# Performance work log

Hardware: AMD Instinct MI355X
Metric: run time of the kernel (lower is better)

Reference implementation:

```python
import jax, jax.numpy as jnp
import numpy as np

V, E, H = 50257, 512, 1024  # vocab, embed_dim, hidden_dim
B, S = 64, 2048             # batch, src_len


def setup_inputs() -> dict:
    key = jax.random.key(0)
    ks = jax.random.split(key, 16)
    sc = 0.02
    emb = jax.random.normal(ks[0], (V, E), jnp.float32) * sc
    emb = emb.at[0].set(0.0)  # padding_idx=0
    return {
        "x": jax.random.randint(ks[1], (B, 1), 0, V),
        "hidden": jax.random.normal(ks[2], (1, B, H), jnp.float32),
        "cell": jax.random.normal(ks[3], (1, B, H), jnp.float32),
        "encoder_outputs": jax.random.normal(ks[4], (B, S, H), jnp.float32),
        "emb": emb,
        "Wa_w": jax.random.normal(ks[5], (H, H), jnp.float32) * sc,
        "Wa_b": jnp.zeros((H,), jnp.float32),
        "Ua_w": jax.random.normal(ks[6], (H, H), jnp.float32) * sc,
        "Ua_b": jnp.zeros((H,), jnp.float32),
        "va_w": jax.random.normal(ks[7], (1, H), jnp.float32) * sc,
        "va_b": jnp.zeros((1,), jnp.float32),
        "Wih": jax.random.normal(ks[8], (4 * H, E + H), jnp.float32) * sc,
        "Whh": jax.random.normal(ks[9], (4 * H, H), jnp.float32) * sc,
        "bih": jnp.zeros((4 * H,), jnp.float32),
        "bhh": jnp.zeros((4 * H,), jnp.float32),
        "fc_w": jax.random.normal(ks[10], (V, H), jnp.float32) * sc,
        "fc_b": jnp.zeros((V,), jnp.float32),
    }


def reference(x, hidden, cell, encoder_outputs, emb, Wa_w, Wa_b, Ua_w, Ua_b,
              va_w, va_b, Wih, Whh, bih, bhh, fc_w, fc_b):
    # Embedding lookup: [B,1] -> [B,E]
    embedded = emb[x[:, 0]]
    # Bahdanau additive attention
    s_t = hidden[-1]                                          # [B,H]
    proj_s = jnp.einsum('bh,oh->bo', s_t, Wa_w) + Wa_b        # [B,H]
    proj_e = jnp.einsum('bsh,oh->bso', encoder_outputs, Ua_w) + Ua_b  # [B,S,H]
    e = jnp.tanh(proj_s[:, None, :] + proj_e)                 # [B,S,H]
    scores = jnp.einsum('bsh,h->bs', e, va_w[0]) + va_b[0]    # [B,S]
    attn = jax.nn.softmax(scores, axis=1)                     # [B,S]
    context = jnp.einsum('bs,bsh->bh', attn, encoder_outputs)  # [B,H]
    # Single-step LSTM (torch gate order: i, f, g, o)
    lstm_in = jnp.concatenate([embedded, context], axis=1)    # [B,E+H]
    gates = lstm_in @ Wih.T + bih + s_t @ Whh.T + bhh         # [B,4H]
    i, f, g, o = jnp.split(gates, 4, axis=1)
    i, f, o = jax.nn.sigmoid(i), jax.nn.sigmoid(f), jax.nn.sigmoid(o)
    g = jnp.tanh(g)
    c_new = f * cell[-1] + i * g
    h_new = o * jnp.tanh(c_new)
    predictions = (h_new @ fc_w.T + fc_b)[:, None, :]          # [B,1,V]
    return predictions, h_new[None], c_new[None]
```

## Files before the change

### kernel.cpp

```cpp
#include <hip/hip_runtime.h>
#include <hip/hip_bf16.h>

#define V_ 50257
#define H_ 1024
#define S_ 2048

typedef float f32x4 __attribute__((ext_vector_type(4)));
typedef short s16x8 __attribute__((ext_vector_type(8)));

__device__ __forceinline__ unsigned short f2bf(float f){
  unsigned u = __builtin_bit_cast(unsigned, f);
  return (unsigned short)((u + 0x7FFFu + ((u >> 16) & 1u)) >> 16);
}
__device__ __forceinline__ unsigned cvt2(float a, float b){
  return (unsigned)f2bf(a) | ((unsigned)f2bf(b) << 16);
}
__device__ __forceinline__ float bf2f(unsigned short h){
  return __builtin_bit_cast(float, (unsigned)h << 16);
}
__device__ __forceinline__ float fast_tanh(float x){
  return 1.0f - 2.0f/(__expf(2.0f*x)+1.0f);
}
__device__ __forceinline__ float fast_sig(float x){
  return 1.0f/(1.0f+__expf(-x));
}
__device__ __forceinline__ void gld_lds16(const void* g, void* l){
  __builtin_amdgcn_global_load_lds((const __attribute__((address_space(1))) void*)g,
                                   (__attribute__((address_space(3))) void*)l, 16, 0, 0);
}

#define BAR() do { __builtin_amdgcn_sched_barrier(0); __builtin_amdgcn_s_barrier(); __builtin_amdgcn_sched_barrier(0); } while(0)
#define VMW8() asm volatile("s_waitcnt vmcnt(8)" ::: "memory")
#define VMW0() asm volatile("s_waitcnt vmcnt(0)" ::: "memory")

__global__ __launch_bounds__(256) void k_cvt_bf16(const float* __restrict__ src,
                                                  unsigned short* __restrict__ dst, int n){
  int i = (blockIdx.x*256 + threadIdx.x)*4;
  if (i < n){
    float4 f = *(const float4*)(src + i);
    uint2 u;
    u.x = cvt2(f.x, f.y);
    u.y = cvt2(f.z, f.w);
    *(uint2*)(dst + i) = u;
  }
}

__global__ __launch_bounds__(256) void k_cvt_enc(const float* __restrict__ src,
                                                 unsigned short* __restrict__ dst){
  const size_t stride = (size_t)gridDim.x * 256;
  const float4* s4 = (const float4*)src;
  uint2* d2 = (uint2*)dst;
  for (size_t i = (size_t)blockIdx.x*256 + threadIdx.x; i < 33554432u; i += stride){
    float4 f = s4[i];
    uint2 u;
    u.x = cvt2(f.x, f.y);
    u.y = cvt2(f.z, f.w);
    d2[i] = u;
  }
}

__global__ __launch_bounds__(512,1) void k_proje256(
    const unsigned short* __restrict__ A,
    const unsigned short* __restrict__ Bw,
    const float* __restrict__ ps,
    const float* __restrict__ Ua_b,
    const float* __restrict__ va,
    float* __restrict__ part)
{
  extern __shared__ unsigned short smem[];
  const int t = threadIdx.x;
  const int lane = t & 63, wid = t >> 6;
  const int lr = lane & 15, lk = lane >> 4;
  const int wr = wid >> 2, wc = wid & 3;

  int bid = blockIdx.x;
  int L = (bid & 7) * 256 + (bid >> 3);
  const int wgm = L >> 2, wgn = L & 3;
  const int m0 = wgm * 256, n0 = wgn * 256;

  const int srow = lane >> 3;
  const int schunk = (lane & 7) ^ srow;

  f32x4 acc[8][4] = {};
  s16x8 af[4], bfr[4];

  auto STAGE = [&](int slot, int kt){
    #pragma unroll
    for (int h = 0; h < 4; ++h){
      const unsigned short* gsrc = (h < 2) ? A : Bw;
      const size_t g0 = (h < 2) ? (size_t)m0 : (size_t)n0;
      unsigned short* ldst = smem + ((h < 2) ? 0 : 32768) + slot*16384;
      #pragma unroll
      for (int j = 0; j < 2; ++j){
        int rb = (h & 1)*128 + j*64 + wid*8;
        gld_lds16(gsrc + (g0 + rb + srow)*1024 + kt*64 + schunk*8,
                  ldst + rb*64);
      }
    }
  };

#define SUBPH(As_, Bs_, msel, ks, LOADB) do { \
    if (LOADB){ \
      _Pragma("unroll") \
      for (int ni = 0; ni < 4; ++ni){ \
        int rl = wc*64 + ni*16 + lr; \
        bfr[ni] = *(const s16x8*)((Bs_) + rl*64 + ((((ks)*4+lk) ^ (lr&7))*8)); \
      } \
    } \
    _Pragma("unroll") \
    for (int mi = 0; mi < 4; ++mi){ \
      int rl = wr*128 + ((msel)*4+mi)*16 + lr; \
      af[mi] = *(const s16x8*)((As_) + rl*64 + ((((ks)*4+lk) ^ (lr&7))*8)); \
    } \
    __builtin_amdgcn_s_setprio(1); \
    _Pragma("unroll") \
    for (int mi = 0; mi < 4; ++mi) \
      _Pragma("unroll") \
      for (int ni = 0; ni < 4; ++ni) \
        acc[(msel)*4+mi][ni] = __builtin_amdgcn_mfma_f32_16x16x32_bf16(af[mi], bfr[ni], acc[(msel)*4+mi][ni], 0,0,0); \
    __builtin_amdgcn_s_setprio(0); \
  } while(0)

#define HALF(slot) do { \
    const unsigned short* As_ = smem + (slot)*16384; \
    const unsigned short* Bs_ = smem + 32768 + (slot)*16384; \
    SUBPH(As_, Bs_, 0, 0, 1); \
    SUBPH(As_, Bs_, 1, 0, 0); \
    SUBPH(As_, Bs_, 0, 1, 1); \
    SUBPH(As_, Bs_, 1, 1, 0); \
  } while(0)

  STAGE(0, 0);
  STAGE(1, 1);
  VMW8(); BAR();

  for (int i = 0; i < 8; ++i){
    HALF(0);
    if (i < 7){
      BAR();
      STAGE(0, 2*i + 2);
      VMW8();
      BAR();
    } else {
      VMW0();
      BAR();
    }
    HALF(1);
    if (i < 7){
      BAR();
      STAGE(1, 2*i + 3);
      VMW8();
      BAR();
    }
  }

  const int b = m0 >> 11;
  float psv[4], vav[4];
  #pragma unroll
  for (int ni = 0; ni < 4; ++ni){
    int n = n0 + wc*64 + ni*16 + lr;
    psv[ni] = ps[b*1024 + n] + Ua_b[n];
    vav[ni] = va[n];
  }
  #pragma unroll
  for (int mi = 0; mi < 8; ++mi){
    float p0=0.f,p1=0.f,p2=0.f,p3=0.f;
    #pragma unroll
    for (int ni = 0; ni < 4; ++ni){
      p0 += vav[ni]*fast_tanh(acc[mi][ni][0] + psv[ni]);
      p1 += vav[ni]*fast_tanh(acc[mi][ni][1] + psv[ni]);
      p2 += vav[ni]*fast_tanh(acc[mi][ni][2] + psv[ni]);
      p3 += vav[ni]*fast_tanh(acc[mi][ni][3] + psv[ni]);
    }
    #pragma unroll
    for (int off = 1; off < 16; off <<= 1){
      p0 += __shfl_xor(p0, off);
      p1 += __shfl_xor(p1, off);
      p2 += __shfl_xor(p2, off);
      p3 += __shfl_xor(p3, off);
    }
    if (lr == 0){
      int rg = m0 + wr*128 + mi*16 + lk*4;
      int slot = wgn*4 + wc;
      part[(size_t)rg*16 + slot]     = p0;
      part[(size_t)(rg+1)*16 + slot] = p1;
      part[(size_t)(rg+2)*16 + slot] = p2;
      part[(size_t)(rg+3)*16 + slot] = p3;
    }
  }
#undef SUBPH
#undef HALF
}

__global__ __launch_bounds__(256,2) void k_proje_f32(
    const float* __restrict__ A,
    const unsigned short* __restrict__ Bw,
    const float* __restrict__ ps,
    const float* __restrict__ Ua_b,
    const float* __restrict__ va,
    float* __restrict__ part)
{
  __shared__ unsigned char sm[32768];
  const int t = threadIdx.x;
  const int lane = t & 63, wid = t >> 6;
  const int lr = lane & 15, lk = lane >> 4;
  int bid = blockIdx.x;
  int L = (bid & 7) * 1024 + (bid >> 3);
  const int wgm = L >> 3, wgn = L & 7;
  const int m0 = wgm * 128, n0 = wgn * 128;
  const int wm = wid >> 1, wn = wid & 1;

  f32x4 acc[4][4] = {};
  const int row2 = t >> 1, half = t & 1;
  const float* aSrc = A + (size_t)(m0 + row2) * 1024 + half * 32;
  const unsigned short* bSrc = Bw + (size_t)(n0 + row2) * 1024 + half * 32;
  unsigned char* Al = sm;
  unsigned char* Bl = sm + 16384;
  const int swzr = row2 & 7;

  for (int kt = 0; kt < 16; ++kt){
    __syncthreads();
    #pragma unroll
    for (int c = 0; c < 4; ++c){
      float4 f0 = *(const float4*)(aSrc + kt*64 + c*8);
      float4 f1 = *(const float4*)(aSrc + kt*64 + c*8 + 4);
      union { unsigned u[4]; s16x8 v; } p;
      p.u[0]=cvt2(f0.x,f0.y); p.u[1]=cvt2(f0.z,f0.w);
      p.u[2]=cvt2(f1.x,f1.y); p.u[3]=cvt2(f1.z,f1.w);
      int ch = half*4 + c;
      *(s16x8*)(Al + row2*128 + ((ch ^ swzr)*16)) = p.v;
    }
    #pragma unroll
    for (int c = 0; c < 4; ++c){
      s16x8 v = *(const s16x8*)(bSrc + kt*64 + (half*4 + c)*8);
      *(s16x8*)(Bl + row2*128 + (((half*4+c) ^ swzr)*16)) = v;
    }
    __syncthreads();
    #pragma unroll
    for (int ks = 0; ks < 2; ++ks){
      s16x8 af[4], bfr[4];
      #pragma unroll
      for (int mi = 0; mi < 4; ++mi){
        int r = wm*64 + mi*16 + lr;
        af[mi] = *(const s16x8*)(Al + r*128 + (((ks*4+lk) ^ (lr&7))*16));
      }
      #pragma unroll
      for (int ni = 0; ni < 4; ++ni){
        int r = wn*64 + ni*16 + lr;
        bfr[ni] = *(const s16x8*)(Bl + r*128 + (((ks*4+lk) ^ (lr&7))*16));
      }
      #pragma unroll
      for (int mi = 0; mi < 4; ++mi)
        #pragma unroll
        for (int ni = 0; ni < 4; ++ni)
          acc[mi][ni] = __builtin_amdgcn_mfma_f32_16x16x32_bf16(af[mi], bfr[ni], acc[mi][ni], 0,0,0);
    }
  }
  const int b = m0 >> 11;
  float psv[4], vav[4];
  #pragma unroll
  for (int ni = 0; ni < 4; ++ni){
    int n = n0 + wn*64 + ni*16 + lr;
    psv[ni] = ps[b*1024 + n] + Ua_b[n];
    vav[ni] = va[n];
  }
  #pragma unroll
  for (int mi = 0; mi < 4; ++mi){
    float p0=0.f,p1=0.f,p2=0.f,p3=0.f;
    #pragma unroll
    for (int ni = 0; ni < 4; ++ni){
      p0 += vav[ni]*fast_tanh(acc[mi][ni][0] + psv[ni]);
      p1 += vav[ni]*fast_tanh(acc[mi][ni][1] + psv[ni]);
      p2 += vav[ni]*fast_tanh(acc[mi][ni][2] + psv[ni]);
      p3 += vav[ni]*fast_tanh(acc[mi][ni][3] + psv[ni]);
    }
    #pragma unroll
    for (int off = 1; off < 16; off <<= 1){
      p0 += __shfl_xor(p0, off);
      p1 += __shfl_xor(p1, off);
      p2 += __shfl_xor(p2, off);
      p3 += __shfl_xor(p3, off);
    }
    if (lr == 0){
      int rg = m0 + wm*64 + mi*16 + lk*4;
      int slot = wgn*2 + wn;
      part[(size_t)rg*16 + slot]     = p0;
      part[(size_t)(rg+1)*16 + slot] = p1;
      part[(size_t)(rg+2)*16 + slot] = p2;
      part[(size_t)(rg+3)*16 + slot] = p3;
    }
  }
}

__global__ __launch_bounds__(256,2) void k_gemm64(
    const float* __restrict__ A,
    const float* __restrict__ B1,
    const float* __restrict__ B2,
    const float* __restrict__ bias1,
    const float* __restrict__ bias2,
    float* __restrict__ C, int ldC,
    int N, int K, int K1)
{
  __shared__ unsigned char sm[16384];
  const int t = threadIdx.x;
  const int lane = t & 63, wid = t >> 6;
  const int lr = lane & 15, lk = lane >> 4;
  const int n0 = blockIdx.x * 64;
  f32x4 acc[4] = {};
  const int row = t >> 2, seg = t & 3;
  unsigned char* Al = sm;
  unsigned char* Bl = sm + 8192;
  const int swzr = row & 7;
  const int K2 = K - K1;

  for (int k0 = 0; k0 < K; k0 += 64){
    __syncthreads();
    {
      const float* s = A + (size_t)row*K + k0 + seg*16;
      #pragma unroll
      for (int c = 0; c < 2; ++c){
        float4 f0 = *(const float4*)(s + c*8);
        float4 f1 = *(const float4*)(s + c*8 + 4);
        union { unsigned u[4]; s16x8 v; } p;
        p.u[0]=cvt2(f0.x,f0.y); p.u[1]=cvt2(f0.z,f0.w);
        p.u[2]=cvt2(f1.x,f1.y); p.u[3]=cvt2(f1.z,f1.w);
        *(s16x8*)(Al + row*128 + (((seg*2+c) ^ swzr)*16)) = p.v;
      }
    }
    {
      int n = n0 + row;
      #pragma unroll
      for (int c = 0; c < 2; ++c){
        union { unsigned u[4]; s16x8 v; } p;
        if (n < N){
          int k = k0 + seg*16 + c*8;
          const float* s;
          if (k < K1) s = B1 + (size_t)n*K1 + k;
          else        s = B2 + (size_t)n*K2 + (k - K1);
          float4 f0 = *(const float4*)(s);
          float4 f1 = *(const float4*)(s + 4);
          p.u[0]=cvt2(f0.x,f0.y); p.u[1]=cvt2(f0.z,f0.w);
          p.u[2]=cvt2(f1.x,f1.y); p.u[3]=cvt2(f1.z,f1.w);
        } else {
          p.u[0]=0u; p.u[1]=0u; p.u[2]=0u; p.u[3]=0u;
        }
        *(s16x8*)(Bl + row*128 + (((seg*2+c) ^ swzr)*16)) = p.v;
      }
    }
    __syncthreads();
    #pragma unroll
    for (int ks = 0; ks < 2; ++ks){
      s16x8 bfr = *(const s16x8*)(Bl + (wid*16+lr)*128 + (((ks*4+lk) ^ (lr&7))*16));
      #pragma unroll
      for (int mi = 0; mi < 4; ++mi){
        s16x8 af = *(const s16x8*)(Al + (mi*16+lr)*128 + (((ks*4+lk) ^ (lr&7))*16));
        acc[mi] = __builtin_amdgcn_mfma_f32_16x16x32_bf16(af, bfr, acc[mi], 0,0,0);
      }
    }
  }
  int n = n0 + wid*16 + lr;
  if (n < N){
    float bv = (bias1 ? bias1[n] : 0.f) + (bias2 ? bias2[n] : 0.f);
    #pragma unroll
    for (int mi = 0; mi < 4; ++mi){
      #pragma unroll
      for (int r = 0; r < 4; ++r){
        C[(size_t)(mi*16 + lk*4 + r)*ldC + n] = acc[mi][r] + bv;
      }
    }
  }
}

__global__ __launch_bounds__(256) void k_softmax(const float* __restrict__ part,
                                                 const float* __restrict__ va_b,
                                                 float* __restrict__ attn){
  __shared__ float sc[2048];
  __shared__ float red[8];
  const int b = blockIdx.x, t = threadIdx.x;
  float vb = va_b[0];
  float lmax = -1e30f;
  #pragma unroll
  for (int j = 0; j < 8; ++j){
    int s = t + j*256;
    const float* p = part + ((size_t)b*2048 + s)*16;
    float v = vb;
    #pragma unroll
    for (int i = 0; i < 16; ++i) v += p[i];
    sc[s] = v;
    lmax = fmaxf(lmax, v);
  }
  for (int off = 32; off; off >>= 1) lmax = fmaxf(lmax, __shfl_xor(lmax, off));
  if ((t&63)==0) red[t>>6] = lmax;
  __syncthreads();
  float m = fmaxf(fmaxf(red[0],red[1]),fmaxf(red[2],red[3]));
  float lsum = 0.f;
  #pragma unroll
  for (int j = 0; j < 8; ++j){
    int s = t + j*256;
    float e = __expf(sc[s]-m);
    sc[s] = e; lsum += e;
  }
  for (int off = 32; off; off >>= 1) lsum += __shfl_xor(lsum, off);
  if ((t&63)==0) red[4 + (t>>6)] = lsum;
  __syncthreads();
  float inv = 1.f/(red[4]+red[5]+red[6]+red[7]);
  #pragma unroll
  for (int j = 0; j < 8; ++j){
    int s = t + j*256;
    attn[(size_t)b*2048+s] = sc[s]*inv;
  }
}

__global__ __launch_bounds__(256) void k_context_bf(const float* __restrict__ attn,
                                                    const unsigned short* __restrict__ encb,
                                                    float* __restrict__ ctxp){
  const int b = blockIdx.x >> 3, scid = blockIdx.x & 7;
  const int t = threadIdx.x;
  float a0=0.f,a1=0.f,a2=0.f,a3=0.f;
  const unsigned short* e = encb + ((size_t)b*2048 + scid*256)*1024 + t*4;
  const float* at = attn + (size_t)b*2048 + scid*256;
  #pragma unroll 4
  for (int s = 0; s < 256; ++s){
    float a = at[s];
    ushort4 v = *(const ushort4*)(e + (size_t)s*1024);
    a0 += a*bf2f(v.x); a1 += a*bf2f(v.y); a2 += a*bf2f(v.z); a3 += a*bf2f(v.w);
  }
  float4 o; o.x=a0; o.y=a1; o.z=a2; o.w=a3;
  *(float4*)(ctxp + ((size_t)scid*64 + b)*1024 + t*4) = o;
}

__global__ __launch_bounds__(256) void k_context_f32(const float* __restrict__ attn,
                                                     const float* __restrict__ enc,
                                                     float* __restrict__ ctxp){
  const int b = blockIdx.x >> 3, scid = blockIdx.x & 7;
  const int t = threadIdx.x;
  float a0=0.f,a1=0.f,a2=0.f,a3=0.f;
  const float* e = enc + ((size_t)b*2048 + scid*256)*1024;
  const float* at = attn + (size_t)b*2048 + scid*256;
  for (int s = 0; s < 256; ++s){
    float a = at[s];
    const float* er = e + (size_t)s*1024;
    a0 += a*er[t]; a1 += a*er[t+256]; a2 += a*er[t+512]; a3 += a*er[t+768];
  }
  float* o = ctxp + ((size_t)scid*64 + b)*1024;
  o[t]=a0; o[t+256]=a1; o[t+512]=a2; o[t+768]=a3;
}

__global__ __launch_bounds__(256) void k_build(const int* __restrict__ x,
                                               const float* __restrict__ emb,
                                               const float* __restrict__ ctxp,
                                               const float* __restrict__ hidden,
                                               float* __restrict__ lstm){
  const int b = blockIdx.x, t = threadIdx.x;
  int xe = x[b];
  for (int col = t; col < 2560; col += 256){
    float v;
    if (col < 512) v = emb[(size_t)xe*512 + col];
    else if (col < 1536){
      int h = col - 512;
      v = 0.f;
      #pragma unroll
      for (int i = 0; i < 8; ++i) v += ctxp[((size_t)i*64 + b)*1024 + h];
    } else v = hidden[(size_t)b*1024 + (col-1536)];
    lstm[(size_t)b*2560 + col] = v;
  }
}

__global__ __launch_bounds__(256) void k_lstm(const float* __restrict__ gates,
                                              const float* __restrict__ cell,
                                              float* __restrict__ out){
  int idx = blockIdx.x*256 + threadIdx.x;
  int b = idx >> 10, h = idx & 1023;
  const float* g = gates + (size_t)b*4096;
  float gi = fast_sig(g[h]);
  float gf = fast_sig(g[h+1024]);
  float gg = fast_tanh(g[h+2048]);
  float go = fast_sig(g[h+3072]);
  float c  = gf*cell[idx] + gi*gg;
  float hn = go*fast_tanh(c);
  out[(size_t)V_*64 + idx]         = hn;
  out[(size_t)V_*64 + 65536 + idx] = c;
}

extern "C" void kernel_launch(void* const* d_in, const int* in_sizes, int n_in,
                              void* d_out, int out_size, void* d_ws, size_t ws_size,
                              hipStream_t stream){
  const int*   x     = (const int*)d_in[0];
  const float* hidden= (const float*)d_in[1];
  const float* cell  = (const float*)d_in[2];
  const float* enc   = (const float*)d_in[3];
  const float* emb   = (const float*)d_in[4];
  const float* Wa_w  = (const float*)d_in[5];
  const float* Wa_b  = (const float*)d_in[6];
  const float* Ua_w  = (const float*)d_in[7];
  const float* Ua_b  = (const float*)d_in[8];
  const float* va_w  = (const float*)d_in[9];
  const float* va_b  = (const float*)d_in[10];
  const float* Wih   = (const float*)d_in[11];
  const float* Whh   = (const float*)d_in[12];
  const float* bih   = (const float*)d_in[13];
  const float* bhh   = (const float*)d_in[14];
  const float* fc_w  = (const float*)d_in[15];
  const float* fc_b  = (const float*)d_in[16];
  float* out = (float*)d_out;
  char* ws = (char*)d_ws;
  unsigned short* ua_bf = (unsigned short*)(ws + 0);
  float* ps    = (float*)(ws + 2097152);
  float* attn  = (float*)(ws + 2359296);
  float* lstm  = (float*)(ws + 2883584);
  float* gates = (float*)(ws + 3538944);
  float* ctxp  = (float*)(ws + 4587520);
  float* part  = (float*)(ws + 6684672);
  unsigned short* enc_bf = (unsigned short*)(ws + 16777216);
  const size_t REQ = 16777216u + 268435456u;

  hipLaunchKernelGGL(k_cvt_bf16, dim3(1024), dim3(256), 0, stream, Ua_w, ua_bf, 1048576);
  hipLaunchKernelGGL(k_gemm64, dim3(16), dim3(256), 0, stream,
                     hidden, Wa_w, nullptr, Wa_b, nullptr, ps, 1024, 1024, 1024, 1024);
  if (ws_size >= REQ){
    hipLaunchKernelGGL(k_cvt_enc, dim3(8192), dim3(256), 0, stream, enc, enc_bf);
    hipLaunchKernelGGL(k_proje256, dim3(2048), dim3(512), 131072, stream,
                       enc_bf, ua_bf, ps, Ua_b, va_w, part);
    hipLaunchKernelGGL(k_softmax, dim3(64), dim3(256), 0, stream, part, va_b, attn);
    hipLaunchKernelGGL(k_context_bf, dim3(512), dim3(256), 0, stream, attn, enc_bf, ctxp);
  } else {
    hipLaunchKernelGGL(k_proje_f32, dim3(8192), dim3(256), 0, stream,
                       enc, ua_bf, ps, Ua_b, va_w, part);
    hipLaunchKernelGGL(k_softmax, dim3(64), dim3(256), 0, stream, part, va_b, attn);
    hipLaunchKernelGGL(k_context_f32, dim3(512), dim3(256), 0, stream, attn, enc, ctxp);
  }
  hipLaunchKernelGGL(k_build, dim3(64), dim3(256), 0, stream, x, emb, ctxp, hidden, lstm);
  hipLaunchKernelGGL(k_gemm64, dim3(64), dim3(256), 0, stream,
                     lstm, Wih, Whh, bih, bhh, gates, 4096, 4096, 2560, 1536);
  hipLaunchKernelGGL(k_lstm, dim3(256), dim3(256), 0, stream, gates, cell, out);
  hipLaunchKernelGGL(k_gemm64, dim3(786), dim3(256), 0, stream,
                     out + (size_t)V_*64, fc_w, nullptr, fc_b, nullptr, out, V_, V_, 1024, 1024);
}
```

Before: 698.9 us.

## Split proje GEMM into two variants, one reading Ua weights directly from global

Splits the attention projection GEMM launch into two halves. The first half keeps the original kernel, which stages both operands into LDS. The second half uses a new variant that stages only the encoder tile in LDS and loads Ua_w fragments straight from global/L2 into registers, using half the shared memory. The context reduction is also split 16 ways over sequence instead of 8, doubling the block count, with the build kernel summing 16 partials and ctxp moved to a larger workspace region. This appears to test whether skipping B staging cuts LDS traffic and barrier cost, at the risk of global-load latency inside the MFMA loop.

Result: slower. 781.5 us (+11.8%).

```diff
diff --git a/kernel.cpp b/kernel.cpp
--- a/kernel.cpp
+++ b/kernel.cpp
@@ -31,6 +31,7 @@
 
 #define BAR() do { __builtin_amdgcn_sched_barrier(0); __builtin_amdgcn_s_barrier(); __builtin_amdgcn_sched_barrier(0); } while(0)
 #define VMW8() asm volatile("s_waitcnt vmcnt(8)" ::: "memory")
+#define VMW4() asm volatile("s_waitcnt vmcnt(4)" ::: "memory")
 #define VMW0() asm volatile("s_waitcnt vmcnt(0)" ::: "memory")
 
 __global__ __launch_bounds__(256) void k_cvt_bf16(const float* __restrict__ src,
@@ -59,13 +60,13 @@
   }
 }
 
-__global__ __launch_bounds__(512,1) void k_proje256(
+__global__ __launch_bounds__(512,1) void k_proje256_a(
     const unsigned short* __restrict__ A,
     const unsigned short* __restrict__ Bw,
     const float* __restrict__ ps,
     const float* __restrict__ Ua_b,
     const float* __restrict__ va,
-    float* __restrict__ part)
+    float* __restrict__ part, int bidBase)
 {
   extern __shared__ unsigned short smem[];
   const int t = threadIdx.x;
@@ -73,7 +74,7 @@
   const int lr = lane & 15, lk = lane >> 4;
   const int wr = wid >> 2, wc = wid & 3;
 
-  int bid = blockIdx.x;
+  int bid = blockIdx.x + bidBase;
   int L = (bid & 7) * 256 + (bid >> 3);
   const int wgm = L >> 2, wgn = L & 3;
   const int m0 = wgm * 256, n0 = wgn * 256;
@@ -192,6 +193,133 @@
 #undef HALF
 }
 
+__global__ __launch_bounds__(512,1) void k_proje256_b(
+    const unsigned short* __restrict__ A,
+    const unsigned short* __restrict__ Bw,
+    const float* __restrict__ ps,
+    const float* __restrict__ Ua_b,
+    const float* __restrict__ va,
+    float* __restrict__ part, int bidBase)
+{
+  extern __shared__ unsigned short smem[];
+  const int t = threadIdx.x;
+  const int lane = t & 63, wid = t >> 6;
+  const int lr = lane & 15, lk = lane >> 4;
+  const int wr = wid >> 2, wc = wid & 3;
+
+  int bid = blockIdx.x + bidBase;
+  int L = (bid & 7) * 256 + (bid >> 3);
+  const int wgm = L >> 2, wgn = L & 3;
+  const int m0 = wgm * 256, n0 = wgn * 256;
+
+  const int srow = lane >> 3;
+  const int schunk = (lane & 7) ^ srow;
+
+  const unsigned short* Bg = Bw + (size_t)n0 * 1024;
+
+  f32x4 acc[8][4] = {};
+  s16x8 af[4], bfr[2][4];
+
+  auto STAGE = [&](int slot, int kt){
+    unsigned short* ldst = smem + slot*16384;
+    #pragma unroll
+    for (int j = 0; j < 4; ++j){
+      int rb = j*64 + wid*8;
+      gld_lds16(A + (size_t)(m0 + rb + srow)*1024 + kt*64 + schunk*8,
+                ldst + rb*64);
+    }
+  };
+
+#define SUBPH_B(As_, msel, ks) do { \
+    _Pragma("unroll") \
+    for (int mi = 0; mi < 4; ++mi){ \
+      int rl = wr*128 + ((msel)*4+mi)*16 + lr; \
+      af[mi] = *(const s16x8*)((As_) + rl*64 + ((((ks)*4+lk) ^ (lr&7))*8)); \
+    } \
+    __builtin_amdgcn_s_setprio(1); \
+    _Pragma("unroll") \
+    for (int mi = 0; mi < 4; ++mi) \
+      _Pragma("unroll") \
+      for (int ni = 0; ni < 4; ++ni) \
+        acc[(msel)*4+mi][ni] = __builtin_amdgcn_mfma_f32_16x16x32_bf16(af[mi], bfr[ks][ni], acc[(msel)*4+mi][ni], 0,0,0); \
+    __builtin_amdgcn_s_setprio(0); \
+  } while(0)
+
+#define HALF_B(slot, kt) do { \
+    const unsigned short* As_ = smem + (slot)*16384; \
+    _Pragma("unroll") \
+    for (int ks2 = 0; ks2 < 2; ++ks2) \
+      _Pragma("unroll") \
+      for (int ni = 0; ni < 4; ++ni) \
+        bfr[ks2][ni] = *(const s16x8*)(Bg + (size_t)(wc*64 + ni*16 + lr)*1024 + (kt)*64 + ks2*32 + lk*8); \
+    SUBPH_B(As_, 0, 0); \
+    SUBPH_B(As_, 1, 0); \
+    SUBPH_B(As_, 0, 1); \
+    SUBPH_B(As_, 1, 1); \
+  } while(0)
+
+  STAGE(0, 0);
+  STAGE(1, 1);
+  VMW4(); BAR();
+
+  for (int i = 0; i < 8; ++i){
+    HALF_B(0, 2*i);
+    if (i < 7){
+      BAR();
+      STAGE(0, 2*i + 2);
+      VMW4();
+      BAR();
+    } else {
+      VMW0();
+      BAR();
+    }
+    HALF_B(1, 2*i + 1);
+    if (i < 7){
+      BAR();
+      STAGE(1, 2*i + 3);
+      VMW4();
+      BAR();
+    }
+  }
+
+  const int b = m0 >> 11;
+  float psv[4], vav[4];
+  #pragma unroll
+  for (int ni = 0; ni < 4; ++ni){
+    int n = n0 + wc*64 + ni*16 + lr;
+    psv[ni] = ps[b*1024 + n] + Ua_b[n];
+    vav[ni] = va[n];
+  }
+  #pragma unroll
+  for (int mi = 0; mi < 8; ++mi){
+    float p0=0.f,p1=0.f,p2=0.f,p3=0.f;
+    #pragma unroll
+    for (int ni = 0; ni < 4; ++ni){
+      p0 += vav[ni]*fast_tanh(acc[mi][ni][0] + psv[ni]);
+      p1 += vav[ni]*fast_tanh(acc[mi][ni][1] + psv[ni]);
+      p2 += vav[ni]*fast_tanh(acc[mi][ni][2] + psv[ni]);
+      p3 += vav[ni]*fast_tanh(acc[mi][ni][3] + psv[ni]);
+    }
+    #pragma unroll
+    for (int off = 1; off < 16; off <<= 1){
+      p0 += __shfl_xor(p0, off);
+      p1 += __shfl_xor(p1, off);
+      p2 += __shfl_xor(p2, off);
+      p3 += __shfl_xor(p3, off);
+    }
+    if (lr == 0){
+      int rg = m0 + wr*128 + mi*16 + lk*4;
+      int slot = wgn*4 + wc;
+      part[(size_t)rg*16 + slot]     = p0;
+      part[(size_t)(rg+1)*16 + slot] = p1;
+      part[(size_t)(rg+2)*16 + slot] = p2;
+      part[(size_t)(rg+3)*16 + slot] = p3;
+    }
+  }
+#undef SUBPH_B
+#undef HALF_B
+}
+
 __global__ __launch_bounds__(256,2) void k_proje_f32(
     const float* __restrict__ A,
     const unsigned short* __restrict__ Bw,
@@ -414,13 +542,13 @@
 __global__ __launch_bounds__(256) void k_context_bf(const float* __restrict__ attn,
                                                     const unsigned short* __restrict__ encb,
                                                     float* __restrict__ ctxp){
-  const int b = blockIdx.x >> 3, scid = blockIdx.x & 7;
+  const int b = blockIdx.x >> 4, scid = blockIdx.x & 15;
   const int t = threadIdx.x;
   float a0=0.f,a1=0.f,a2=0.f,a3=0.f;
-  const unsigned short* e = encb + ((size_t)b*2048 + scid*256)*1024 + t*4;
-  const float* at = attn + (size_t)b*2048 + scid*256;
+  const unsigned short* e = encb + ((size_t)b*2048 + scid*128)*1024 + t*4;
+  const float* at = attn + (size_t)b*2048 + scid*128;
   #pragma unroll 4
-  for (int s = 0; s < 256; ++s){
+  for (int s = 0; s < 128; ++s){
     float a = at[s];
     ushort4 v = *(const ushort4*)(e + (size_t)s*1024);
     a0 += a*bf2f(v.x); a1 += a*bf2f(v.y); a2 += a*bf2f(v.z); a3 += a*bf2f(v.w);
@@ -432,12 +560,12 @@
 __global__ __launch_bounds__(256) void k_context_f32(const float* __restrict__ attn,
                                                      const float* __restrict__ enc,
                                                      float* __restrict__ ctxp){
-  const int b = blockIdx.x >> 3, scid = blockIdx.x & 7;
+  const int b = blockIdx.x >> 4, scid = blockIdx.x & 15;
   const int t = threadIdx.x;
   float a0=0.f,a1=0.f,a2=0.f,a3=0.f;
-  const float* e = enc + ((size_t)b*2048 + scid*256)*1024;
-  const float* at = attn + (size_t)b*2048 + scid*256;
-  for (int s = 0; s < 256; ++s){
+  const float* e = enc + ((size_t)b*2048 + scid*128)*1024;
+  const float* at = attn + (size_t)b*2048 + scid*128;
+  for (int s = 0; s < 128; ++s){
     float a = at[s];
     const float* er = e + (size_t)s*1024;
     a0 += a*er[t]; a1 += a*er[t+256]; a2 += a*er[t+512]; a3 += a*er[t+768];
@@ -460,7 +588,7 @@
       int h = col - 512;
       v = 0.f;
       #pragma unroll
-      for (int i = 0; i < 8; ++i) v += ctxp[((size_t)i*64 + b)*1024 + h];
+      for (int i = 0; i < 16; ++i) v += ctxp[((size_t)i*64 + b)*1024 + h];
     } else v = hidden[(size_t)b*1024 + (col-1536)];
     lstm[(size_t)b*2560 + col] = v;
   }
@@ -509,8 +637,8 @@
   float* attn  = (float*)(ws + 2359296);
   float* lstm  = (float*)(ws + 2883584);
   float* gates = (float*)(ws + 3538944);
-  float* ctxp  = (float*)(ws + 4587520);
   float* part  = (float*)(ws + 6684672);
+  float* ctxp  = (float*)(ws + 10878976);
   unsigned short* enc_bf = (unsigned short*)(ws + 16777216);
   const size_t REQ = 16777216u + 268435456u;
 
@@ -519,15 +647,17 @@
                      hidden, Wa_w, nullptr, Wa_b, nullptr, ps, 1024, 1024, 1024, 1024);
   if (ws_size >= REQ){
     hipLaunchKernelGGL(k_cvt_enc, dim3(8192), dim3(256), 0, stream, enc, enc_bf);
-    hipLaunchKernelGGL(k_proje256, dim3(2048), dim3(512), 131072, stream,
-                       enc_bf, ua_bf, ps, Ua_b, va_w, part);
+    hipLaunchKernelGGL(k_proje256_a, dim3(1024), dim3(512), 131072, stream,
+                       enc_bf, ua_bf, ps, Ua_b, va_w, part, 0);
+    hipLaunchKernelGGL(k_proje256_b, dim3(1024), dim3(512), 65536, stream,
+                       enc_bf, ua_bf, ps, Ua_b, va_w, part, 1024);
     hipLaunchKernelGGL(k_softmax, dim3(64), dim3(256), 0, stream, part, va_b, attn);
-    hipLaunchKernelGGL(k_context_bf, dim3(512), dim3(256), 0, stream, attn, enc_bf, ctxp);
+    hipLaunchKernelGGL(k_context_bf, dim3(1024), dim3(256), 0, stream, attn, enc_bf, ctxp);
   } else {
     hipLaunchKernelGGL(k_proje_f32, dim3(8192), dim3(256), 0, stream,
                        enc, ua_bf, ps, Ua_b, va_w, part);
     hipLaunchKernelGGL(k_softmax, dim3(64), dim3(256), 0, stream, part, va_b, attn);
-    hipLaunchKernelGGL(k_context_f32, dim3(512), dim3(256), 0, stream, attn, enc, ctxp);
+    hipLaunchKernelGGL(k_context_f32, dim3(1024), dim3(256), 0, stream, attn, enc, ctxp);
   }
   hipLaunchKernelGGL(k_build, dim3(64), dim3(256), 0, stream, x, emb, ctxp, hidden, lstm);
   hipLaunchKernelGGL(k_gemm64, dim3(64), dim3(256), 0, stream,
```
